# Kernel optimization log

Measured on AMD Instinct MI355X. Metric: run time of the kernel, lower is better.

## Reference

```python
import jax, jax.numpy as jnp
import numpy as np

DIM = 1024
HEADS = 8
EV = DIM  # dim*expand - dim with expand=2
P = 2.0   # power-softmax exponent
EPS = 1e-5


def setup_inputs() -> dict:
    key = jax.random.key(0)
    k1, k2, k3 = jax.random.split(key, 3)
    B, L = 4, 2048
    x = jax.random.normal(k1, (B, L, DIM), dtype=jnp.float32)
    gamma = jnp.ones((DIM,), dtype=jnp.float32)
    beta = jnp.zeros((DIM,), dtype=jnp.float32)
    # torch nn.Linear weights are [out_features, in_features]
    w_qkv = jax.random.normal(k2, (5 * DIM, DIM), dtype=jnp.float32) * (DIM ** -0.5)
    w_out = jax.random.normal(k3, (DIM, 2 * DIM), dtype=jnp.float32) * ((2 * DIM) ** -0.5)
    return {"x": x, "gamma": gamma, "beta": beta, "w_qkv": w_qkv, "w_out": w_out}


def _layernorm(x, gamma, beta):
    xf = x.astype(jnp.float32)
    mu = jnp.mean(xf, axis=-1, keepdims=True)
    var = jnp.mean(jnp.square(xf - mu), axis=-1, keepdims=True)
    return ((xf - mu) * jax.lax.rsqrt(var + EPS)) * gamma + beta


def _p_softmax(scores, scale, p):
    # scores: [B,H,L,L] with -inf on masked entries
    s = scores.astype(jnp.float32) * scale
    if p == 1.0:
        return jax.nn.softmax(s, axis=-1)
    lse = jax.nn.logsumexp(s * p, axis=-1, keepdims=True) / p
    return jnp.exp(s - lse)


def _attention(q, k, v, heads, p):
    B, L, D = q.shape
    hd = D // heads
    q = q.reshape(B, L, heads, hd).transpose(0, 2, 1, 3)  # bhld
    k = k.reshape(B, L, heads, hd).transpose(0, 2, 1, 3)
    v = v.reshape(B, L, heads, hd).transpose(0, 2, 1, 3)
    scores = jnp.einsum('bhqd,bhkd->bhqk', q, k)
    mask = jnp.tril(jnp.ones((L, L), dtype=bool))
    scores = jnp.where(mask, scores, -jnp.inf)
    probs = _p_softmax(scores, hd ** -0.5, p).astype(q.dtype)
    out = jnp.einsum('bhqk,bhkd->bhqd', probs, v)
    return out.transpose(0, 2, 1, 3).reshape(B, L, D)


def reference(x, gamma, beta, w_qkv, w_out):
    h = _layernorm(x, gamma, beta).astype(x.dtype)
    proj = h @ w_qkv.T  # [B,L,5*DIM]
    q, k, v, lin, pre = jnp.split(proj, np.cumsum([DIM, DIM, DIM, EV]), axis=-1)
    attn = _attention(q, k, v, HEADS, P)
    branch = jnp.concatenate([lin * jax.nn.gelu(pre, approximate=False), attn], axis=-1)
    return x + branch @ w_out.T
```

## Files before the change

kernel.cpp:

```cpp
#include <hip/hip_runtime.h>
#include <hip/hip_bf16.h>
#include <math.h>

#define DIMD 1024
#define LSEQ 2048
#define BATCH 4
#define NHEAD 8
#define HD 128
#define NROWS (BATCH*LSEQ)
#define PROJC (5*DIMD)
#define BRC (2*DIMD)

typedef __attribute__((ext_vector_type(8))) short short8;
typedef __attribute__((ext_vector_type(4))) short short4v;
typedef __attribute__((ext_vector_type(4))) float floatx4;

__device__ __forceinline__ float bf2f(short s) {
  unsigned int u = ((unsigned int)(unsigned short)s) << 16;
  return __builtin_bit_cast(float, u);
}
__device__ __forceinline__ short f2bf(float f) {
  unsigned int u = __builtin_bit_cast(unsigned int, f);
  unsigned int lsb = (u >> 16) & 1u;
  u += 0x7fffu + lsb;
  return (short)(u >> 16);
}

__device__ __forceinline__ void gl2lds16(const short* g, short* l) {
  __builtin_amdgcn_global_load_lds(
      (const __attribute__((address_space(1))) unsigned int*)(unsigned long long)g,
      (__attribute__((address_space(3))) unsigned int*)(unsigned int)(unsigned long long)l,
      16, 0, 0);
}

__device__ __forceinline__ void wgbar() {
  asm volatile("" ::: "memory");
  __builtin_amdgcn_s_barrier();
  asm volatile("" ::: "memory");
}

__global__ __launch_bounds__(256) void pre_kernel(
    const float* __restrict__ x, const float* __restrict__ gamma,
    const float* __restrict__ beta, short* __restrict__ h,
    const float* __restrict__ s1, short* __restrict__ d1, int n1_4,
    const float* __restrict__ s2, short* __restrict__ d2, int n2_4,
    int nblk_cvt) {
  int bid = blockIdx.x;
  if (bid < nblk_cvt) {
    int i = bid * 256 + threadIdx.x;
    const float* src; short* dst;
    if (i < n1_4) { src = s1; dst = d1; }
    else { i -= n1_4; if (i >= n2_4) return; src = s2; dst = d2; }
    float4 v = *(const float4*)(src + (size_t)i * 4);
    short4v o;
    o[0] = f2bf(v.x); o[1] = f2bf(v.y); o[2] = f2bf(v.z); o[3] = f2bf(v.w);
    *(short4v*)(dst + (size_t)i * 4) = o;
    return;
  }
  int row = bid - nblk_cvt;
  int c = threadIdx.x * 4;
  const float* xr = x + (size_t)row * DIMD;
  float4 v = *(const float4*)(xr + c);
  float f[4] = {v.x, v.y, v.z, v.w};
  float sum = 0.f, sq = 0.f;
  for (int i = 0; i < 4; ++i) { sum += f[i]; sq += f[i]*f[i]; }
  for (int off = 1; off < 64; off <<= 1) {
    sum += __shfl_xor(sum, off);
    sq  += __shfl_xor(sq, off);
  }
  __shared__ float red[8];
  int wid = threadIdx.x >> 6;
  if ((threadIdx.x & 63) == 0) { red[wid*2] = sum; red[wid*2+1] = sq; }
  __syncthreads();
  sum = red[0]+red[2]+red[4]+red[6];
  sq  = red[1]+red[3]+red[5]+red[7];
  float mu = sum * (1.0f/DIMD);
  float var = sq * (1.0f/DIMD) - mu*mu;
  float rstd = rsqrtf(var + 1e-5f);
  float4 g = *(const float4*)(gamma + c);
  float4 bb = *(const float4*)(beta + c);
  float gg[4] = {g.x, g.y, g.z, g.w};
  float bv[4] = {bb.x, bb.y, bb.z, bb.w};
  short4v o;
  for (int i = 0; i < 4; ++i)
    o[i] = f2bf((f[i] - mu) * rstd * gg[i] + bv[i]);
  *(short4v*)(h + (size_t)row * DIMD + c) = o;
}

__device__ __forceinline__ void rd_a(const short* base, int s0, int s1,
                                     short8 (&a)[4][2]) {
#pragma unroll
  for (int m = 0; m < 4; ++m) {
    a[m][0] = *(const short8*)(base + m*16*64 + s0);
    a[m][1] = *(const short8*)(base + m*16*64 + s1);
  }
}
__device__ __forceinline__ void rd_b(const short* base, int s0, int s1,
                                     short8 (&b)[2][2]) {
#pragma unroll
  for (int n = 0; n < 2; ++n) {
    b[n][0] = *(const short8*)(base + n*16*64 + s0);
    b[n][1] = *(const short8*)(base + n*16*64 + s1);
  }
}
template<int QM, int QN>
__device__ __forceinline__ void qmm(const short8 (&a)[4][2], const short8 (&b)[2][2],
                                    floatx4 (&acc)[8][4]) {
  __builtin_amdgcn_s_setprio(1);
#pragma unroll
  for (int m = 0; m < 4; ++m)
#pragma unroll
    for (int n = 0; n < 2; ++n) {
      floatx4 c = acc[QM*4+m][QN*2+n];
      c = __builtin_amdgcn_mfma_f32_16x16x32_bf16(a[m][0], b[n][0], c, 0, 0, 0);
      c = __builtin_amdgcn_mfma_f32_16x16x32_bf16(a[m][1], b[n][1], c, 0, 0, 0);
      acc[QM*4+m][QN*2+n] = c;
    }
  __builtin_amdgcn_s_setprio(0);
}
template<int QN>
__device__ __forceinline__ void qmm2(const short8 (&a)[4][2], const short8 (&b)[2][2],
                                     floatx4 (&acc)[4][4]) {
  __builtin_amdgcn_s_setprio(1);
#pragma unroll
  for (int m = 0; m < 4; ++m)
#pragma unroll
    for (int n = 0; n < 2; ++n) {
      floatx4 c = acc[m][QN*2+n];
      c = __builtin_amdgcn_mfma_f32_16x16x32_bf16(a[m][0], b[n][0], c, 0, 0, 0);
      c = __builtin_amdgcn_mfma_f32_16x16x32_bf16(a[m][1], b[n][1], c, 0, 0, 0);
      acc[m][QN*2+n] = c;
    }
  __builtin_amdgcn_s_setprio(0);
}
__device__ __forceinline__ void stg2(const short* p, int K, short* lds) {
  gl2lds16(p, lds);
  gl2lds16(p + (size_t)64*K, lds + 64*64);
}
__device__ __forceinline__ void stg4(const short* p, int K, short* lds, int koff) {
  stg2(p + koff, K, lds);
  stg2(p + (size_t)128*K + koff, K, lds + 128*64);
}

__global__ __launch_bounds__(512, 2) void gemm256(const short* __restrict__ A,
    const short* __restrict__ W, short* __restrict__ C, short* __restrict__ VT,
    int M, int N, int K) {
  __shared__ __align__(16) short AsF[2*256*64];
  __shared__ __align__(16) short WsF[2*256*64];
  const int tid = threadIdx.x;
  const int lane = tid & 63, wv = tid >> 6;
  const int wm = wv >> 2, wn = wv & 3;
  const int quad = lane >> 4, l16 = lane & 15;

  const int nbx = N >> 8;
  int cpx = gridDim.x >> 3;
  int orig = blockIdx.x;
  int wg = (orig & 7) * cpx + (orig >> 3);
  int bx = wg % nbx, by = wg / nbx;
  const int row0 = by << 8, col0 = bx << 8;

  const int lrow = lane >> 3;
  const int sslot = (lane & 7) ^ lrow;
  const short* pA = A + (size_t)(row0 + wv*8 + lrow) * K + sslot*8;
  const short* pW = W + (size_t)(col0 + wv*8 + lrow) * K + sslot*8;
  short* stA = AsF + wv*8*64;
  short* stW = WsF + wv*8*64;
  const short* aB = AsF + (wm*128 + l16)*64;
  const short* wB = WsF + (wn*64 + l16)*64;
  const int s0 = (quad ^ (l16 & 7)) << 3;
  const int s1 = s0 ^ 32;

  floatx4 acc[8][4] = {};
  short8 a[4][2], b0[2][2], b1[2][2];

  const int nktm = (K >> 6) - 1;

  stg4(pA, K, stA, 0);
  stg4(pW, K, stW, 0);
  stg4(pA, K, stA + 16384, 64);
  asm volatile("s_waitcnt vmcnt(4)" ::: "memory");
  wgbar();

  const int NT = K >> 6;
  for (int t = 0; t < NT; ++t) {
    const int cur = (t & 1) << 14;
    const int nxt = cur ^ 16384;
    const int kw1 = ((t + 1) & nktm) << 6;
    const int ka2 = ((t + 2) & nktm) << 6;
    rd_a(aB + cur, s0, s1, a);
    rd_b(wB + cur, s0, s1, b0);
    stg4(pW, K, stW + nxt, kw1);
    wgbar();
    qmm<0,0>(a, b0, acc);
    rd_b(wB + cur + 32*64, s0, s1, b1);
    wgbar();
    qmm<0,1>(a, b1, acc);
    rd_a(aB + cur + 64*64, s0, s1, a);
    wgbar();
    qmm<1,1>(a, b1, acc);
    wgbar();
    stg4(pA, K, stA + cur, ka2);
    qmm<1,0>(a, b0, acc);
    asm volatile("s_waitcnt vmcnt(4)" ::: "memory");
    wgbar();
  }
  asm volatile("s_waitcnt vmcnt(0)" ::: "memory");

  const bool isV = (col0 >= 2*DIMD) && (col0 < 3*DIMD);
  if (!isV) {
#pragma unroll
    for (int i = 0; i < 8; ++i) {
      int r0 = row0 + wm*128 + i*16 + quad*4;
#pragma unroll
      for (int j = 0; j < 4; ++j) {
        int cc = col0 + wn*64 + j*16 + l16;
#pragma unroll
        for (int r = 0; r < 4; ++r)
          C[(size_t)(r0 + r) * N + cc] = f2bf(acc[i][j][r]);
      }
    }
  } else {
    int grow = row0 + wm*128;
    int bb = grow >> 11, lbase = grow & 2047;
#pragma unroll
    for (int j = 0; j < 4; ++j) {
      int dg = col0 - 2*DIMD + wn*64 + j*16 + l16;
      short* dcol = VT + (((size_t)(bb*NHEAD + (dg >> 7))*HD + (dg & 127))*LSEQ
                          + lbase + quad*4);
#pragma unroll
      for (int i = 0; i < 8; ++i) {
        short4v p;
#pragma unroll
        for (int r = 0; r < 4; ++r) p[r] = f2bf(acc[i][j][r]);
        *(short4v*)(dcol + i*16) = p;
      }
    }
  }
}

__global__ __launch_bounds__(512, 2) void gemm2(const short* __restrict__ A,
    const short* __restrict__ W, const float* __restrict__ X,
    float* __restrict__ out, int M, int N, int K) {
  __shared__ __align__(16) short As2[2*128*64];
  __shared__ __align__(16) short Ws2[2*256*64];
  const int tid = threadIdx.x;
  const int lane = tid & 63, wv = tid >> 6;
  const int wm = wv >> 2, wn = wv & 3;
  const int quad = lane >> 4, l16 = lane & 15;

  const int nbx = N >> 8;
  int cpx = gridDim.x >> 3;
  int orig = blockIdx.x;
  int wg = (orig & 7) * cpx + (orig >> 3);
  int bx = wg % nbx, by = wg / nbx;
  const int row0 = by << 7, col0 = bx << 8;

  const int lrow = lane >> 3;
  const int sslot = (lane & 7) ^ lrow;
  const short* pA = A + (size_t)(row0 + wv*8 + lrow) * K + sslot*8;
  const short* pW = W + (size_t)(col0 + wv*8 + lrow) * K + sslot*8;
  short* stA = As2 + wv*8*64;
  short* stW = Ws2 + wv*8*64;
  const short* aB = As2 + (wm*64 + l16)*64;
  const short* wB = Ws2 + (wn*64 + l16)*64;
  const int s0 = (quad ^ (l16 & 7)) << 3;
  const int s1 = s0 ^ 32;

  floatx4 acc[4][4] = {};
  short8 a[4][2], b0[2][2], b1[2][2];

  const int nktm = (K >> 6) - 1;

  stg2(pA, K, stA);
  stg4(pW, K, stW, 0);
  stg2(pA + 64, K, stA + 8192);
  asm volatile("s_waitcnt vmcnt(2)" ::: "memory");
  wgbar();

  const int NT = K >> 6;
  for (int t = 0; t < NT; ++t) {
    const int curA = (t & 1) << 13;
    const int curW = (t & 1) << 14;
    const int nxtW = curW ^ 16384;
    const int kw1 = ((t + 1) & nktm) << 6;
    const int ka2 = ((t + 2) & nktm) << 6;
    rd_a(aB + curA, s0, s1, a);
    rd_b(wB + curW, s0, s1, b0);
    stg4(pW, K, stW + nxtW, kw1);
    wgbar();
    qmm2<0>(a, b0, acc);
    rd_b(wB + curW + 32*64, s0, s1, b1);
    wgbar();
    stg2(pA + ka2, K, stA + curA);
    qmm2<1>(a, b1, acc);
    asm volatile("s_waitcnt vmcnt(2)" ::: "memory");
    wgbar();
  }
  asm volatile("s_waitcnt vmcnt(0)" ::: "memory");

#pragma unroll
  for (int i = 0; i < 4; ++i) {
    int r0 = row0 + wm*64 + i*16 + quad*4;
#pragma unroll
    for (int j = 0; j < 4; ++j) {
      int cc = col0 + wn*64 + j*16 + l16;
#pragma unroll
      for (int r = 0; r < 4; ++r) {
        size_t idx = (size_t)(r0 + r) * N + cc;
        out[idx] = acc[i][j][r] + X[idx];
      }
    }
  }
}

__global__ __launch_bounds__(256) void gelu_kernel(const short* __restrict__ proj,
    short* __restrict__ branch) {
  int row = blockIdx.x;
  int c = threadIdx.x * 4;
  const short* pr = proj + (size_t)row * PROJC;
  short4v lin = *(const short4v*)(pr + 3*DIMD + c);
  short4v pre = *(const short4v*)(pr + 4*DIMD + c);
  short4v o;
  for (int i = 0; i < 4; ++i) {
    float xx = bf2f(pre[i]);
    float g = 0.5f * xx * (1.f + erff(xx * 0.70710678118654752f));
    o[i] = f2bf(bf2f(lin[i]) * g);
  }
  *(short4v*)(branch + (size_t)row * BRC + c) = o;
}

__global__ __launch_bounds__(512) void attn_kernel(const short* __restrict__ proj,
    const short* __restrict__ vt, short* __restrict__ branch) {
  int bh = blockIdx.y;
  int b = bh >> 3, hh = bh & 7;
  int gx = blockIdx.x;
  int gsel = (bh < 16) ? gx : (15 - gx);
  int tid = threadIdx.x;
  int wv = tid >> 6, lane = tid & 63, quad = lane >> 4, l16 = lane & 15;
  int qsel = 2*gsel + ((wv < 4) ? 0 : 1);
  int qw = qsel * 64 + (wv & 3) * 16;

  const short* Qp  = proj + (size_t)b * LSEQ * PROJC + hh*HD;
  const short* Kp  = Qp + DIMD;
  const short* VTp = vt + (size_t)bh * HD * LSEQ;

  __shared__ short Ks[64][136];
  __shared__ short Vs[128][76];
  __shared__ short Ps[8][16][44];

  short8 qf[4];
  {
    const short* qrow = Qp + (size_t)(qw + l16) * PROJC;
    for (int s = 0; s < 4; ++s) qf[s] = *(const short8*)(qrow + s*32 + quad*8);
  }
  float lsum[4] = {0.f, 0.f, 0.f, 0.f};
  floatx4 O[8] = {};

  const float scale = 0.08838834764831845f;
  int NT = 2*gsel + 2;
  int krow = tid >> 4;
  int kcol = (tid & 15) * 8;
  int vd = tid >> 2;
  int vk = (tid & 3) * 8;

  short8 kv0 = *(const short8*)(Kp + (size_t)(krow) * PROJC + kcol);
  short8 kv1 = *(const short8*)(Kp + (size_t)(32 + krow) * PROJC + kcol);
  short8 vv0 = *(const short8*)(VTp + (size_t)vd * LSEQ + vk);
  short8 vv1 = *(const short8*)(VTp + (size_t)vd * LSEQ + 32 + vk);

  for (int kt = 0; kt < NT; ++kt) {
    int kb64 = kt * 64;
    __syncthreads();
    *(short8*)&Ks[krow][kcol]      = kv0;
    *(short8*)&Ks[krow + 32][kcol] = kv1;
    *(short8*)&Vs[vd][vk]          = vv0;
    *(short8*)&Vs[vd][32 + vk]     = vv1;
    {
      int ktn = (kt + 1 < NT) ? (kt + 1) : kt;
      int kb64n = ktn * 64;
      kv0 = *(const short8*)(Kp + (size_t)(kb64n + krow) * PROJC + kcol);
      kv1 = *(const short8*)(Kp + (size_t)(kb64n + 32 + krow) * PROJC + kcol);
      vv0 = *(const short8*)(VTp + (size_t)vd * LSEQ + kb64n + vk);
      vv1 = *(const short8*)(VTp + (size_t)vd * LSEQ + kb64n + 32 + vk);
    }
    __syncthreads();
    for (int hf = 0; hf < 2; ++hf) {
      int kb = kb64 + hf*32;
      if (kb <= qw + 15) {
        floatx4 s0 = {0.f,0.f,0.f,0.f}, s1 = {0.f,0.f,0.f,0.f};
        __builtin_amdgcn_s_setprio(1);
        for (int s = 0; s < 4; ++s) {
          short8 kf0 = *(const short8*)&Ks[hf*32 + l16][s*32 + quad*8];
          short8 kf1 = *(const short8*)&Ks[hf*32 + 16 + l16][s*32 + quad*8];
          s0 = __builtin_amdgcn_mfma_f32_16x16x32_bf16(qf[s], kf0, s0, 0, 0, 0);
          s1 = __builtin_amdgcn_mfma_f32_16x16x32_bf16(qf[s], kf1, s1, 0, 0, 0);
        }
        __builtin_amdgcn_s_setprio(0);
        int c0 = kb + l16, c1 = kb + 16 + l16;
        for (int r = 0; r < 4; ++r) {
          int q = qw + quad*4 + r;
          float w0 = (c0 <= q) ? __expf(s0[r] * scale) : 0.f;
          float w1 = (c1 <= q) ? __expf(s1[r] * scale) : 0.f;
          lsum[r] += w0*w0 + w1*w1;
          Ps[wv][quad*4+r][l16]      = f2bf(w0);
          Ps[wv][quad*4+r][16 + l16] = f2bf(w1);
        }
        asm volatile("s_waitcnt lgkmcnt(0)" ::: "memory");
        short8 pf = *(const short8*)&Ps[wv][l16][quad*8];
        __builtin_amdgcn_s_setprio(1);
        for (int t8 = 0; t8 < 8; ++t8) {
          short8 vf = *(const short8*)&Vs[t8*16 + l16][hf*32 + quad*8];
          O[t8] = __builtin_amdgcn_mfma_f32_16x16x32_bf16(pf, vf, O[t8], 0, 0, 0);
        }
        __builtin_amdgcn_s_setprio(0);
      }
    }
  }
  for (int r = 0; r < 4; ++r) {
    float l = lsum[r];
    for (int off = 1; off < 16; off <<= 1) l += __shfl_xor(l, off);
    float inv = rsqrtf(l);
    int q = qw + quad*4 + r;
    short* orow = branch + ((size_t)(b*LSEQ + q)) * BRC + DIMD + hh*HD;
    for (int t8 = 0; t8 < 8; ++t8)
      orow[t8*16 + l16] = f2bf(O[t8][r] * inv);
  }
}

extern "C" void kernel_launch(void* const* d_in, const int* in_sizes, int n_in,
                              void* d_out, int out_size, void* d_ws, size_t ws_size,
                              hipStream_t stream) {
  const float* x     = (const float*)d_in[0];
  const float* gamma = (const float*)d_in[1];
  const float* beta  = (const float*)d_in[2];
  const float* w_qkv = (const float*)d_in[3];
  const float* w_out = (const float*)d_in[4];
  float* out = (float*)d_out;

  char* ws = (char*)d_ws;
  short* h      = (short*)ws;
  short* proj   = (short*)(ws + (size_t)16*1024*1024);
  short* branch = (short*)(ws + (size_t)96*1024*1024);
  short* wq     = (short*)(ws + (size_t)128*1024*1024);
  short* wo     = (short*)(ws + (size_t)138*1024*1024);
  short* vt     = (short*)out;

  int n1 = PROJC*DIMD/4, n2 = DIMD*BRC/4;
  int nblk_cvt = (n1 + n2 + 255)/256;
  pre_kernel<<<nblk_cvt + NROWS, 256, 0, stream>>>(x, gamma, beta, h,
                                                   w_qkv, wq, n1, w_out, wo, n2,
                                                   nblk_cvt);
  gemm256<<<dim3((NROWS/256)*(PROJC/256)), 512, 0, stream>>>(h, wq, proj, vt,
                                                             NROWS, PROJC, DIMD);
  gelu_kernel<<<NROWS, 256, 0, stream>>>(proj, branch);
  attn_kernel<<<dim3(16, BATCH*NHEAD), 512, 0, stream>>>(proj, vt, branch);
  gemm2<<<dim3(256), 512, 0, stream>>>(branch, wo, x, out, NROWS, DIMD, BRC);
}
```

Before: 315.3 us.

## Fuse GELU gating into QKV projection GEMM epilogue and drop gelu kernel

```diff
diff --git a/kernel.cpp b/kernel.cpp
--- a/kernel.cpp
+++ b/kernel.cpp
@@ -137,16 +137,18 @@
   gl2lds16(p, lds);
   gl2lds16(p + (size_t)64*K, lds + 64*64);
 }
-__device__ __forceinline__ void stg4(const short* p, int K, short* lds, int koff) {
-  stg2(p + koff, K, lds);
-  stg2(p + (size_t)128*K + koff, K, lds + 128*64);
+__device__ __forceinline__ void stg4b(const short* p0, const short* p1, int K,
+                                      short* lds, int koff) {
+  stg2(p0 + koff, K, lds);
+  stg2(p1 + koff, K, lds + 128*64);
 }
 
 __global__ __launch_bounds__(512, 2) void gemm256(const short* __restrict__ A,
     const short* __restrict__ W, short* __restrict__ C, short* __restrict__ VT,
-    int M, int N, int K) {
-  __shared__ __align__(16) short AsF[2*256*64];
-  __shared__ __align__(16) short WsF[2*256*64];
+    short* __restrict__ BR, int M, int N, int K) {
+  __shared__ __align__(16) short SH[4*256*64];
+  short* AsF = SH;
+  short* WsF = SH + 2*256*64;
   const int tid = threadIdx.x;
   const int lane = tid & 63, wv = tid >> 6;
   const int wm = wv >> 2, wn = wv & 3;
@@ -158,11 +160,16 @@
   int wg = (orig & 7) * cpx + (orig >> 3);
   int bx = wg % nbx, by = wg / nbx;
   const int row0 = by << 8, col0 = bx << 8;
+  const int blkty = (bx >= 12) ? 2 : ((bx >= 8) ? 1 : 0);
+  const int c0 = (bx - 12) << 7;
 
   const int lrow = lane >> 3;
   const int sslot = (lane & 7) ^ lrow;
-  const short* pA = A + (size_t)(row0 + wv*8 + lrow) * K + sslot*8;
-  const short* pW = W + (size_t)(col0 + wv*8 + lrow) * K + sslot*8;
+  const int wr0 = (blkty == 2) ? (3*DIMD + c0) : col0;
+  const int wr1 = (blkty == 2) ? (4*DIMD + c0) : (col0 + 128);
+  const short* pA  = A + (size_t)(row0 + wv*8 + lrow) * K + sslot*8;
+  const short* pW  = W + (size_t)(wr0 + wv*8 + lrow) * K + sslot*8;
+  const short* pW2 = W + (size_t)(wr1 + wv*8 + lrow) * K + sslot*8;
   short* stA = AsF + wv*8*64;
   short* stW = WsF + wv*8*64;
   const short* aB = AsF + (wm*128 + l16)*64;
@@ -175,9 +182,9 @@
 
   const int nktm = (K >> 6) - 1;
 
-  stg4(pA, K, stA, 0);
-  stg4(pW, K, stW, 0);
-  stg4(pA, K, stA + 16384, 64);
+  stg4b(pA, pA + (size_t)128*K, K, stA, 0);
+  stg4b(pW, pW2, K, stW, 0);
+  stg4b(pA, pA + (size_t)128*K, K, stA + 16384, 64);
   asm volatile("s_waitcnt vmcnt(4)" ::: "memory");
   wgbar();
 
@@ -189,7 +196,7 @@
     const int ka2 = ((t + 2) & nktm) << 6;
     rd_a(aB + cur, s0, s1, a);
     rd_b(wB + cur, s0, s1, b0);
-    stg4(pW, K, stW + nxt, kw1);
+    stg4b(pW, pW2, K, stW + nxt, kw1);
     wgbar();
     qmm<0,0>(a, b0, acc);
     rd_b(wB + cur + 32*64, s0, s1, b1);
@@ -199,15 +206,14 @@
     wgbar();
     qmm<1,1>(a, b1, acc);
     wgbar();
-    stg4(pA, K, stA + cur, ka2);
+    stg4b(pA + ka2, pA + (size_t)128*K + ka2, K, stA + cur, 0);
     qmm<1,0>(a, b0, acc);
     asm volatile("s_waitcnt vmcnt(4)" ::: "memory");
     wgbar();
   }
   asm volatile("s_waitcnt vmcnt(0)" ::: "memory");
 
-  const bool isV = (col0 >= 2*DIMD) && (col0 < 3*DIMD);
-  if (!isV) {
+  if (blkty == 0) {
 #pragma unroll
     for (int i = 0; i < 8; ++i) {
       int r0 = row0 + wm*128 + i*16 + quad*4;
@@ -219,7 +225,7 @@
           C[(size_t)(r0 + r) * N + cc] = f2bf(acc[i][j][r]);
       }
     }
-  } else {
+  } else if (blkty == 1) {
     int grow = row0 + wm*128;
     int bb = grow >> 11, lbase = grow & 2047;
 #pragma unroll
@@ -233,6 +239,42 @@
 #pragma unroll
         for (int r = 0; r < 4; ++r) p[r] = f2bf(acc[i][j][r]);
         *(short4v*)(dcol + i*16) = p;
+      }
+    }
+  } else {
+    wgbar();
+    short* G = SH;
+    if ((wn & 2) == 0) {
+      int colb = wn*64;
+#pragma unroll
+      for (int i = 0; i < 8; ++i) {
+        int row = wm*128 + i*16 + quad*4;
+#pragma unroll
+        for (int j = 0; j < 4; ++j) {
+          int cl = colb + j*16 + l16;
+#pragma unroll
+          for (int r = 0; r < 4; ++r)
+            G[(row + r)*132 + cl] = f2bf(acc[i][j][r]);
+        }
+      }
+    }
+    wgbar();
+    if (wn & 2) {
+      int colb = (wn - 2)*64;
+#pragma unroll
+      for (int i = 0; i < 8; ++i) {
+        int row = wm*128 + i*16 + quad*4;
+#pragma unroll
+        for (int j = 0; j < 4; ++j) {
+          int cl = colb + j*16 + l16;
+#pragma unroll
+          for (int r = 0; r < 4; ++r) {
+            float pre = bf2f(f2bf(acc[i][j][r]));
+            float g = 0.5f * pre * (1.f + erff(pre * 0.70710678118654752f));
+            float lin = bf2f(G[(row + r)*132 + cl]);
+            BR[(size_t)(row0 + row + r) * BRC + c0 + cl] = f2bf(lin * g);
+          }
+        }
       }
     }
   }
@@ -272,7 +314,8 @@
   const int nktm = (K >> 6) - 1;
 
   stg2(pA, K, stA);
-  stg4(pW, K, stW, 0);
+  stg2(pW, K, stW);
+  stg2(pW + (size_t)128*K, K, stW + 128*64);
   stg2(pA + 64, K, stA + 8192);
   asm volatile("s_waitcnt vmcnt(2)" ::: "memory");
   wgbar();
@@ -286,7 +329,8 @@
     const int ka2 = ((t + 2) & nktm) << 6;
     rd_a(aB + curA, s0, s1, a);
     rd_b(wB + curW, s0, s1, b0);
-    stg4(pW, K, stW + nxtW, kw1);
+    stg2(pW + kw1, K, stW + nxtW);
+    stg2(pW + (size_t)128*K + kw1, K, stW + nxtW + 128*64);
     wgbar();
     qmm2<0>(a, b0, acc);
     rd_b(wB + curW + 32*64, s0, s1, b1);
@@ -311,22 +355,6 @@
       }
     }
   }
-}
-
-__global__ __launch_bounds__(256) void gelu_kernel(const short* __restrict__ proj,
-    short* __restrict__ branch) {
-  int row = blockIdx.x;
-  int c = threadIdx.x * 4;
-  const short* pr = proj + (size_t)row * PROJC;
-  short4v lin = *(const short4v*)(pr + 3*DIMD + c);
-  short4v pre = *(const short4v*)(pr + 4*DIMD + c);
-  short4v o;
-  for (int i = 0; i < 4; ++i) {
-    float xx = bf2f(pre[i]);
-    float g = 0.5f * xx * (1.f + erff(xx * 0.70710678118654752f));
-    o[i] = f2bf(bf2f(lin[i]) * g);
-  }
-  *(short4v*)(branch + (size_t)row * BRC + c) = o;
 }
 
 __global__ __launch_bounds__(512) void attn_kernel(const short* __restrict__ proj,
@@ -451,8 +479,8 @@
                                                    w_qkv, wq, n1, w_out, wo, n2,
                                                    nblk_cvt);
   gemm256<<<dim3((NROWS/256)*(PROJC/256)), 512, 0, stream>>>(h, wq, proj, vt,
+                                                             branch,
                                                              NROWS, PROJC, DIMD);
-  gelu_kernel<<<NROWS, 256, 0, stream>>>(proj, branch);
   attn_kernel<<<dim3(16, BATCH*NHEAD), 512, 0, stream>>>(proj, vt, branch);
   gemm2<<<dim3(256), 512, 0, stream>>>(branch, wo, x, out, NROWS, DIMD, BRC);
 }
```

Result: slower. 340.8 us (+8.1%).
